# Kernel tuning notes

Measured on AMD Instinct MI355X. Metric: run time of the kernel, lower is better.

Reference implementation:

```python
import jax, jax.numpy as jnp
import numpy as np

LOG_2PIE = float(np.log(2 * np.pi * np.e))


def _mu_logvar(inputs, targets, W_fe, b_fe, W_lv, b_lv):
    # inputs: [Nep, N, Din], targets: [Nep, N, 1]
    phis = jax.nn.relu(jnp.einsum('end,df->enf', inputs, W_fe) + b_fe)  # [Nep, N, D]
    x = jnp.concatenate([targets, phis], axis=-1)                        # [Nep, N, D+1]
    # z = cat(mean over shots, std over shots (unbiased, as torch.std))
    z = jnp.concatenate([jnp.mean(x, axis=1), jnp.std(x, axis=1, ddof=1)], axis=-1)  # [Nep, T]
    mu = z  # use_net_for_mu=False
    logvar = jnp.clip(z @ W_lv + b_lv, -9.0, -2.0)  # Linear + Hardtanh(-9,-2)
    return mu, logvar


def _pairwise_kl(mu1, lv1, mu2, lv2):
    # KL(N(mu1_i, lv1_i) || N(mu2_j, lv2_j)) for all (i, j): [Nep, Nep]
    m1, l1 = mu1[:, None, :], lv1[:, None, :]
    m2, l2 = mu2[None, :, :], lv2[None, :, :]
    t = l2 - l1 + (jnp.exp(l1) + (m1 - m2) ** 2) * jnp.exp(-l2) - 1.0
    return 0.5 * jnp.sum(t, axis=-1)


def reference(train_inputs, train_targets, test_inputs, test_targets, W_fe, b_fe, W_lv, b_lv):
    mu_tr, lv_tr = _mu_logvar(train_inputs, train_targets, W_fe, b_fe, W_lv, b_lv)
    mu_te, lv_te = _mu_logvar(test_inputs, test_targets, W_fe, b_fe, W_lv, b_lv)
    T = mu_tr.shape[-1]
    # normal_entropy as written in source: logvar.sum() + 0.5*d*log(2*pi*e)
    H_tr = jnp.sum(lv_tr, axis=-1) + 0.5 * T * LOG_2PIE  # [Nep]
    H_te = jnp.sum(lv_te, axis=-1) + 0.5 * T * LOG_2PIE  # [Nep]
    score = (_pairwise_kl(mu_tr, lv_tr, mu_te, lv_te)
             + _pairwise_kl(mu_te, lv_te, mu_tr, lv_tr).T
             + H_tr[:, None] + H_te[None, :])
    probs = jax.nn.log_softmax(-score, axis=1)
    classes = jnp.arange(score.shape[0], dtype=jnp.int64 if jax.config.jax_enable_x64 else jnp.int32)
    return probs, classes


def setup_inputs() -> dict:
    key = jax.random.key(0)
    ks = jax.random.split(key, 6)
    Nep, N, Din, D = 256, 32, 512, 512
    T = 2 * (D + 1)
    return {
        'train_inputs': jax.random.normal(ks[0], (Nep, N, Din), jnp.float32),
        'train_targets': jax.random.normal(ks[1], (Nep, N, 1), jnp.float32),
        'test_inputs': jax.random.normal(ks[2], (Nep, N, Din), jnp.float32),
        'test_targets': jax.random.normal(ks[3], (Nep, N, 1), jnp.float32),
        'W_fe': jax.random.normal(ks[4], (Din, D), jnp.float32) / np.sqrt(Din),
        'b_fe': jnp.zeros((D,), jnp.float32),
        'W_lv': jax.random.normal(ks[5], (T, T), jnp.float32) / np.sqrt(T),
        'b_lv': jnp.zeros((T,), jnp.float32),
    }
```

## Files before the change

kernel.cpp:

```cpp
#include <hip/hip_runtime.h>
#include <math.h>

#define TDIM 1026
#define KP 1056
#define NP 1152
#define KSPLIT 7
#define KK 4224

typedef __attribute__((ext_vector_type(8))) short bf16x8;
typedef __attribute__((ext_vector_type(4))) float f32x4;

__device__ inline unsigned int pk_bf16(float a, float b) {
    unsigned int ua = __float_as_uint(a), ub = __float_as_uint(b);
    ua = (ua + 0x7FFFu + ((ua >> 16) & 1u)) >> 16;
    ub = (ub + 0x7FFFu + ((ub >> 16) & 1u)) & 0xFFFF0000u;
    return ua | ub;
}
__device__ inline unsigned short f2bf(float a) {
    unsigned int ua = __float_as_uint(a);
    return (unsigned short)((ua + 0x7FFFu + ((ua >> 16) & 1u)) >> 16);
}

__global__ __launch_bounds__(256)
void k_cvtboth(const float* __restrict__ Wfe, const float* __restrict__ Wlv,
               unsigned short* __restrict__ Wt, unsigned short* __restrict__ Wlt)
{
    __shared__ float T[32][33];
    const int z = blockIdx.z;
    if (z && (blockIdx.x >= 16 || blockIdx.y >= 16)) return;
    const float* W = z ? Wfe : Wlv;
    unsigned short* D = z ? Wt : Wlt;
    const int S  = z ? 512 : TDIM;
    const int DS = z ? 512 : KP;
    const int n0 = blockIdx.x * 32, k0 = blockIdx.y * 32;
    const int t = threadIdx.x;
    {
        int ky = t >> 3, nx = (t & 7) * 4;
#pragma unroll
        for (int i = 0; i < 4; ++i) {
            float v = 0.f;
            if (k0 + ky < S && n0 + nx + i < S)
                v = W[(size_t)(k0 + ky) * S + n0 + nx + i];
            T[nx + i][ky] = v;
        }
    }
    __syncthreads();
    {
        int ny = t >> 3, kx = (t & 7) * 4;
        ushort4 o;
        o.x = f2bf(T[ny][kx + 0]); o.y = f2bf(T[ny][kx + 1]);
        o.z = f2bf(T[ny][kx + 2]); o.w = f2bf(T[ny][kx + 3]);
        *(ushort4*)(D + (size_t)(n0 + ny) * DS + k0 + kx) = o;
    }
}

__global__ __launch_bounds__(256)
void k_fe_mfma(const float* __restrict__ Atr, const float* __restrict__ Ate,
               const unsigned short* __restrict__ Wt,
               const float* __restrict__ bfe, float* __restrict__ Z,
               unsigned short* __restrict__ Zb)
{
    __shared__ unsigned short As[64 * 40];
    __shared__ unsigned short Bs[128 * 40];
    __shared__ float2 sbuf[2 * 128];

    const int tid  = threadIdx.x;
    const int lane = tid & 63;
    const int wave = tid >> 6;
    const int m = lane & 15, quad = lane >> 4;
    const int row0 = blockIdx.x * 64;
    const int col0 = blockIdx.y * 128;
    const float* A = (row0 < 8192) ? Atr : Ate;
    const int ar0 = row0 & 8191;

    f32x4 acc[4][2];
#pragma unroll
    for (int i = 0; i < 4; ++i)
#pragma unroll
        for (int j = 0; j < 2; ++j) acc[i][j] = (f32x4){0.f, 0.f, 0.f, 0.f};

    const int srA = tid >> 2, skA = tid & 3;
    const int srB = tid >> 1, skB = tid & 1;

    float4 pa0, pa1;
    uint4  pb0, pb1;

#define FE_PRELOAD(K0)                                                          \
    {                                                                           \
        const float* ap = A + (size_t)(ar0 + srA) * 512 + (K0) + skA * 8;       \
        pa0 = *(const float4*)(ap);                                             \
        pa1 = *(const float4*)(ap + 4);                                         \
        const unsigned short* bp = Wt + (size_t)(col0 + srB) * 512 + (K0) + skB * 16; \
        pb0 = *(const uint4*)(bp);                                              \
        pb1 = *(const uint4*)(bp + 8);                                          \
    }

    FE_PRELOAD(0)
    for (int k0 = 0; k0 < 512; k0 += 32) {
        __syncthreads();
        {
            uint4 va;
            va.x = pk_bf16(pa0.x, pa0.y); va.y = pk_bf16(pa0.z, pa0.w);
            va.z = pk_bf16(pa1.x, pa1.y); va.w = pk_bf16(pa1.z, pa1.w);
            *(uint4*)(As + srA * 40 + skA * 8) = va;
            *(uint4*)(Bs + srB * 40 + skB * 16)     = pb0;
            *(uint4*)(Bs + srB * 40 + skB * 16 + 8) = pb1;
        }
        __syncthreads();
        if (k0 + 32 < 512) FE_PRELOAD(k0 + 32)
        bf16x8 af[4], bfr[2];
#pragma unroll
        for (int ti = 0; ti < 4; ++ti)
            af[ti] = *(const bf16x8*)(As + (ti * 16 + m) * 40 + quad * 8);
#pragma unroll
        for (int tj = 0; tj < 2; ++tj)
            bfr[tj] = *(const bf16x8*)(Bs + (wave * 32 + tj * 16 + m) * 40 + quad * 8);
#pragma unroll
        for (int ti = 0; ti < 4; ++ti)
#pragma unroll
            for (int tj = 0; tj < 2; ++tj)
                acc[ti][tj] = __builtin_amdgcn_mfma_f32_16x16x32_bf16(
                    af[ti], bfr[tj], acc[ti][tj], 0, 0, 0);
    }

#pragma unroll
    for (int ep = 0; ep < 2; ++ep) {
#pragma unroll
        for (int tj = 0; tj < 2; ++tj) {
            int colL = wave * 32 + tj * 16 + m;
            float b = bfe[col0 + colL];
            float s1 = 0.f, s2 = 0.f;
#pragma unroll
            for (int p = 0; p < 2; ++p) {
                int ti = ep * 2 + p;
#pragma unroll
                for (int r = 0; r < 4; ++r) {
                    float v = fmaxf(acc[ti][tj][r] + b, 0.f);
                    s1 += v; s2 += v * v;
                }
            }
            s1 += __shfl_xor(s1, 16); s1 += __shfl_xor(s1, 32);
            s2 += __shfl_xor(s2, 16); s2 += __shfl_xor(s2, 32);
            if (lane < 16) sbuf[ep * 128 + colL] = make_float2(s1, s2);
        }
    }
    __syncthreads();
    {
        int ep = tid >> 7, cl = tid & 127;
        float2 pr = sbuf[ep * 128 + cl];
        float mean = pr.x * (1.f / 32.f);
        float var  = (pr.y - 32.f * mean * mean) * (1.f / 31.f);
        float sd   = sqrtf(fmaxf(var, 0.f));
        int e = blockIdx.x * 2 + ep;
        int f = col0 + cl;
        Z[(size_t)e * TDIM + 1 + f]   = mean;
        Z[(size_t)e * TDIM + 514 + f] = sd;
        Zb[(size_t)e * KP + 1 + f]    = f2bf(mean);
        Zb[(size_t)e * KP + 514 + f]  = f2bf(sd);
    }
}

__global__ __launch_bounds__(256)
void k_tgt(const float* __restrict__ Ttr, const float* __restrict__ Tte,
           float* __restrict__ Z, unsigned short* __restrict__ Zb,
           float* __restrict__ Hs_te, float* __restrict__ cterm)
{
    if (blockIdx.x == 0) { Hs_te[threadIdx.x] = 0.f; cterm[threadIdx.x] = 0.f; }
    int e = blockIdx.x * 256 + threadIdx.x;
    if (e >= 512) return;
    const float* p = (e < 256) ? (Ttr + (size_t)e * 32) : (Tte + (size_t)(e - 256) * 32);
    float S1 = 0.f, S2 = 0.f;
#pragma unroll
    for (int n = 0; n < 32; ++n) { float v = p[n]; S1 += v; S2 += v * v; }
    float mean = S1 * (1.f / 32.f);
    float var  = (S2 - 32.f * mean * mean) * (1.f / 31.f);
    float sd   = sqrtf(fmaxf(var, 0.f));
    Z[(size_t)e * TDIM + 0]   = mean;
    Z[(size_t)e * TDIM + 513] = sd;
    Zb[(size_t)e * KP + 0]    = f2bf(mean);
    Zb[(size_t)e * KP + 513]  = f2bf(sd);
#pragma unroll
    for (int c = TDIM; c < KP; ++c) Zb[(size_t)e * KP + c] = 0;
}

__global__ __launch_bounds__(256)
void k_lv_mfma(const unsigned short* __restrict__ Zb,
               const unsigned short* __restrict__ Wlt,
               float* __restrict__ Cacc)
{
    __shared__ unsigned short As[128 * 40];
    __shared__ unsigned short Bs[128 * 40];

    const int tid  = threadIdx.x;
    const int lane = tid & 63;
    const int wave = tid >> 6;
    const int wr = wave >> 1, wc = wave & 1;
    const int m = lane & 15, quad = lane >> 4;
    const int col0 = blockIdx.x * 128;
    const int row0 = blockIdx.y * 128;
    const int p    = blockIdx.z;
    const int it0  = (p < 5) ? p * 5 : 25 + (p - 5) * 4;
    const int itn  = (p < 5) ? 5 : 4;

    f32x4 acc[4][4];
#pragma unroll
    for (int i = 0; i < 4; ++i)
#pragma unroll
        for (int j = 0; j < 4; ++j) acc[i][j] = (f32x4){0.f, 0.f, 0.f, 0.f};

    const int srow = tid >> 2;
    const int skc  = tid & 3;

    for (int it = it0; it < it0 + itn; ++it) {
        int k0 = it * 32;
#pragma unroll
        for (int s = 0; s < 2; ++s) {
            int row = srow + s * 64;
            uint4 va = *(const uint4*)(Zb  + (size_t)(row0 + row) * KP + k0 + skc * 8);
            uint4 vb = *(const uint4*)(Wlt + (size_t)(col0 + row) * KP + k0 + skc * 8);
            *(uint4*)(As + row * 40 + skc * 8) = va;
            *(uint4*)(Bs + row * 40 + skc * 8) = vb;
        }
        __syncthreads();
        bf16x8 af[4], bfr[4];
#pragma unroll
        for (int t2 = 0; t2 < 4; ++t2) {
            af[t2]  = *(const bf16x8*)(As + (wr * 64 + t2 * 16 + m) * 40 + quad * 8);
            bfr[t2] = *(const bf16x8*)(Bs + (wc * 64 + t2 * 16 + m) * 40 + quad * 8);
        }
#pragma unroll
        for (int ti = 0; ti < 4; ++ti)
#pragma unroll
            for (int tj = 0; tj < 4; ++tj)
                acc[ti][tj] = __builtin_amdgcn_mfma_f32_16x16x32_bf16(
                    af[ti], bfr[tj], acc[ti][tj], 0, 0, 0);
        __syncthreads();
    }

    float* C = Cacc + (size_t)p * 512 * NP;
#pragma unroll
    for (int ti = 0; ti < 4; ++ti)
#pragma unroll
        for (int tj = 0; tj < 4; ++tj) {
            int c = col0 + wc * 64 + tj * 16 + m;
#pragma unroll
            for (int r = 0; r < 4; ++r) {
                int rg = row0 + wr * 64 + ti * 16 + quad * 4 + r;
                C[(size_t)rg * NP + c] = acc[ti][tj][r];
            }
        }
}

__global__ __launch_bounds__(256)
void k_lv_ep(const float* __restrict__ Cacc, const float* __restrict__ Zf,
             const float* __restrict__ blv,
             unsigned short* __restrict__ Xb, unsigned short* __restrict__ Yb,
             float* __restrict__ Hs_te, float* __restrict__ cterm)
{
    const int t = threadIdx.x;
    const int rl = t >> 3;
    const int ci = t & 7;
    const int r  = blockIdx.y * 32 + rl;
    const int c0 = blockIdx.x * 32 + ci * 4;
    const bool is_te = (r >= 256);

    float4 s = make_float4(0.f, 0.f, 0.f, 0.f);
#pragma unroll
    for (int p = 0; p < KSPLIT; ++p) {
        float4 v = *(const float4*)(Cacc + (size_t)p * 512 * NP + (size_t)r * NP + c0);
        s.x += v.x; s.y += v.y; s.z += v.z; s.w += v.w;
    }
    float sv[4] = {s.x, s.y, s.z, s.w};

    unsigned short* O = is_te ? (Yb + (size_t)(r - 256) * KK) : (Xb + (size_t)r * KK);
    float h = 0.f, ct = 0.f;
#pragma unroll
    for (int q = 0; q < 4; ++q) {
        int c = c0 + q;
        bool cok = (c < TDIM);
        ushort4 o = make_ushort4(0, 0, 0, 0);
        if (cok) {
            float x = fminf(fmaxf(sv[q] + blv[c], -9.f), -2.f);
            float E = expf(x);
            float R = expf(-x);
            float mm = Zf[(size_t)r * TDIM + c];
            if (!is_te) {
                o.x = f2bf(E + mm * mm);
                o.y = f2bf(R);
                o.z = f2bf(-2.f * mm * R);
                o.w = f2bf(-2.f * mm);
            } else {
                o.x = f2bf(R);
                o.y = f2bf(E + mm * mm);
                o.z = f2bf(mm);
                o.w = f2bf(mm * R);
                h  += x;
                ct += mm * mm * R;
            }
        }
        *(ushort4*)(O + 4 * c) = o;
    }
    if (is_te) {
        h  += __shfl_xor(h, 1);  h  += __shfl_xor(h, 2);  h  += __shfl_xor(h, 4);
        ct += __shfl_xor(ct, 1); ct += __shfl_xor(ct, 2); ct += __shfl_xor(ct, 4);
        if (ci == 0) {
            atomicAdd(Hs_te + (r - 256), h);
            atomicAdd(cterm + (r - 256), ct);
        }
    }
}

__global__ __launch_bounds__(256)
void k_pgemm(const unsigned short* __restrict__ Xb,
             const unsigned short* __restrict__ Yb,
             float* __restrict__ Sp)
{
    __shared__ unsigned short As[128 * 40];
    __shared__ unsigned short Bs[128 * 40];

    const int tid  = threadIdx.x;
    const int lane = tid & 63;
    const int wave = tid >> 6;
    const int wr = wave >> 1, wc = wave & 1;
    const int m = lane & 15, quad = lane >> 4;
    const int col0 = blockIdx.x * 128;
    const int row0 = blockIdx.y * 128;
    const int p    = blockIdx.z;
    const int it0  = (p < 4) ? p * 9 : 36 + (p - 4) * 8;
    const int itn  = (p < 4) ? 9 : 8;

    f32x4 acc[4][4];
#pragma unroll
    for (int i = 0; i < 4; ++i)
#pragma unroll
        for (int j = 0; j < 4; ++j) acc[i][j] = (f32x4){0.f, 0.f, 0.f, 0.f};

    const int srow = tid >> 2;
    const int skc  = tid & 3;

    for (int it = it0; it < it0 + itn; ++it) {
        int k0 = it * 32;
#pragma unroll
        for (int s = 0; s < 2; ++s) {
            int row = srow + s * 64;
            uint4 va = *(const uint4*)(Xb + (size_t)(row0 + row) * KK + k0 + skc * 8);
            uint4 vb = *(const uint4*)(Yb + (size_t)(col0 + row) * KK + k0 + skc * 8);
            *(uint4*)(As + row * 40 + skc * 8) = va;
            *(uint4*)(Bs + row * 40 + skc * 8) = vb;
        }
        __syncthreads();
        bf16x8 af[4], bfr[4];
#pragma unroll
        for (int t2 = 0; t2 < 4; ++t2) {
            af[t2]  = *(const bf16x8*)(As + (wr * 64 + t2 * 16 + m) * 40 + quad * 8);
            bfr[t2] = *(const bf16x8*)(Bs + (wc * 64 + t2 * 16 + m) * 40 + quad * 8);
        }
#pragma unroll
        for (int ti = 0; ti < 4; ++ti)
#pragma unroll
            for (int tj = 0; tj < 4; ++tj)
                acc[ti][tj] = __builtin_amdgcn_mfma_f32_16x16x32_bf16(
                    af[ti], bfr[tj], acc[ti][tj], 0, 0, 0);
        __syncthreads();
    }

    float* C = Sp + (size_t)p * 65536;
#pragma unroll
    for (int ti = 0; ti < 4; ++ti)
#pragma unroll
        for (int tj = 0; tj < 4; ++tj) {
            int c = col0 + wc * 64 + tj * 16 + m;
#pragma unroll
            for (int r = 0; r < 4; ++r) {
                int rg = row0 + wr * 64 + ti * 16 + quad * 4 + r;
                C[(size_t)rg * 256 + c] = acc[ti][tj][r];
            }
        }
}

__global__ __launch_bounds__(256)
void k_soft(const float* __restrict__ Sp, const float* __restrict__ Hs_te,
            const float* __restrict__ cterm, float* __restrict__ outp)
{
    __shared__ float red[4], red2[4];
    const int i = blockIdx.x, j = threadIdx.x;
    float s = 0.f;
#pragma unroll
    for (int tc = 0; tc < 16; ++tc)
        s += Sp[((size_t)tc * 256 + i) * 256 + j];
    float v = -(0.5f * (s + cterm[j]) + Hs_te[j]);

    float m = v;
#pragma unroll
    for (int o = 32; o > 0; o >>= 1) m = fmaxf(m, __shfl_xor(m, o));
    if ((j & 63) == 0) red[j >> 6] = m;
    __syncthreads();
    m = fmaxf(fmaxf(red[0], red[1]), fmaxf(red[2], red[3]));

    float p = v - m;
    float t = expf(p);
#pragma unroll
    for (int o = 32; o > 0; o >>= 1) t += __shfl_xor(t, o);
    if ((j & 63) == 0) red2[j >> 6] = t;
    __syncthreads();
    t = red2[0] + red2[1] + red2[2] + red2[3];

    outp[(size_t)i * 256 + j] = p - logf(t);
    if (i == 0) outp[65536 + j] = (float)j;
}

__global__ __launch_bounds__(256)
void k_fe_f32(const float* __restrict__ Atr, const float* __restrict__ Ate,
              const float* __restrict__ Wfe, const float* __restrict__ bfe,
              float* __restrict__ Z, float* __restrict__ muT_te)
{
    __shared__ float lds[4224];
    float* Ast = lds;
    float* Bs  = lds + 2112;
    const int tid = threadIdx.x;
    const int tx = tid & 15;
    const int ty = tid >> 4;
    const int col0 = blockIdx.x * 128;
    const int row0 = blockIdx.y * 128;
    const float* A = (row0 < 8192) ? Atr : Ate;
    const int ar0 = (row0 < 8192) ? row0 : (row0 - 8192);

    float acc[8][8];
#pragma unroll
    for (int i = 0; i < 8; ++i)
#pragma unroll
        for (int j = 0; j < 8; ++j) acc[i][j] = 0.f;

    for (int k0 = 0; k0 < 512; k0 += 16) {
#pragma unroll
        for (int s = 0; s < 2; ++s) {
            int u = tid + s * 256;
            int row = u >> 2, q = u & 3;
            float4 v = *(const float4*)(A + (size_t)(ar0 + row) * 512 + k0 + q * 4);
            Ast[(q * 4 + 0) * 132 + row] = v.x;
            Ast[(q * 4 + 1) * 132 + row] = v.y;
            Ast[(q * 4 + 2) * 132 + row] = v.z;
            Ast[(q * 4 + 3) * 132 + row] = v.w;
        }
#pragma unroll
        for (int s = 0; s < 2; ++s) {
            int u = tid + s * 256;
            int kk = u >> 5, c8 = u & 31;
            float4 v = *(const float4*)(Wfe + (size_t)(k0 + kk) * 512 + col0 + c8 * 4);
            *(float4*)(Bs + kk * 132 + c8 * 4) = v;
        }
        __syncthreads();
#pragma unroll
        for (int kk = 0; kk < 16; ++kk) {
            float4 a0 = *(const float4*)(Ast + kk * 132 + ty * 8);
            float4 a1 = *(const float4*)(Ast + kk * 132 + ty * 8 + 4);
            float4 b0 = *(const float4*)(Bs + kk * 132 + tx * 4);
            float4 b1 = *(const float4*)(Bs + kk * 132 + 64 + tx * 4);
            float av[8] = {a0.x, a0.y, a0.z, a0.w, a1.x, a1.y, a1.z, a1.w};
            float bv[8] = {b0.x, b0.y, b0.z, b0.w, b1.x, b1.y, b1.z, b1.w};
#pragma unroll
            for (int i = 0; i < 8; ++i)
#pragma unroll
                for (int j = 0; j < 8; ++j)
                    acc[i][j] = fmaf(av[i], bv[j], acc[i][j]);
        }
        __syncthreads();
    }

    float2* sbuf = (float2*)lds;
#pragma unroll
    for (int j = 0; j < 8; ++j) {
        int cl = (j < 4) ? (tx * 4 + j) : (64 + tx * 4 + (j - 4));
        float b = bfe[col0 + cl];
        float s1 = 0.f, s2 = 0.f;
#pragma unroll
        for (int i = 0; i < 8; ++i) {
            float v = acc[i][j] + b;
            v = fmaxf(v, 0.f);
            s1 += v; s2 += v * v;
        }
        sbuf[ty * 128 + cl] = make_float2(s1, s2);
    }
    __syncthreads();
    for (int idx = tid; idx < 512; idx += 256) {
        int ep = idx >> 7, cl = idx & 127;
        float S1 = 0.f, S2 = 0.f;
#pragma unroll
        for (int q = 0; q < 4; ++q) {
            float2 p = sbuf[(ep * 4 + q) * 128 + cl];
            S1 += p.x; S2 += p.y;
        }
        float mean = S1 * (1.f / 32.f);
        float var  = (S2 - 32.f * mean * mean) * (1.f / 31.f);
        float sd   = sqrtf(fmaxf(var, 0.f));
        int e = (row0 >> 5) + ep;
        int f = col0 + cl;
        Z[(size_t)e * TDIM + 1 + f]   = mean;
        Z[(size_t)e * TDIM + 514 + f] = sd;
        if (e >= 256) {
            int j2 = e - 256;
            muT_te[(size_t)(1 + f) * 256 + j2]   = mean;
            muT_te[(size_t)(514 + f) * 256 + j2] = sd;
        }
    }
}

__global__ __launch_bounds__(256)
void k_tgt_f32(const float* __restrict__ Ttr, const float* __restrict__ Tte,
               float* __restrict__ Z, float* __restrict__ muT_te,
               float* __restrict__ Hs_te)
{
    if (blockIdx.x == 0) Hs_te[threadIdx.x] = 0.f;
    int e = blockIdx.x * 256 + threadIdx.x;
    if (e >= 512) return;
    const float* p = (e < 256) ? (Ttr + (size_t)e * 32) : (Tte + (size_t)(e - 256) * 32);
    float S1 = 0.f, S2 = 0.f;
#pragma unroll
    for (int n = 0; n < 32; ++n) { float v = p[n]; S1 += v; S2 += v * v; }
    float mean = S1 * (1.f / 32.f);
    float var  = (S2 - 32.f * mean * mean) * (1.f / 31.f);
    float sd   = sqrtf(fmaxf(var, 0.f));
    Z[(size_t)e * TDIM + 0]   = mean;
    Z[(size_t)e * TDIM + 513] = sd;
    if (e >= 256) {
        muT_te[(size_t)0 * 256 + (e - 256)]   = mean;
        muT_te[(size_t)513 * 256 + (e - 256)] = sd;
    }
}

__global__ __launch_bounds__(256)
void k_lv(const float* __restrict__ Z, const float* __restrict__ Wlv,
          const float* __restrict__ blv,
          float* __restrict__ E_tr, float* __restrict__ R_tr,
          float* __restrict__ E_teT, float* __restrict__ R_teT,
          float* __restrict__ Hs_te)
{
    __shared__ float Ast[16 * 68];
    __shared__ float Bs[16 * 68];
    const int tid = threadIdx.x;
    const int tx = tid & 15;
    const int ty = tid >> 4;
    const int col0 = blockIdx.x * 64;
    const int row0 = blockIdx.y * 64;

    float acc[4][4];
#pragma unroll
    for (int i = 0; i < 4; ++i)
#pragma unroll
        for (int j = 0; j < 4; ++j) acc[i][j] = 0.f;

    for (int k0 = 0; k0 < TDIM; k0 += 16) {
        {
            int row = tid >> 2, kp = tid & 3;
            const float* src = Z + (size_t)(row0 + row) * TDIM + k0 + kp * 4;
            float x0 = 0.f, x1 = 0.f, x2 = 0.f, x3 = 0.f;
            if (k0 + kp * 4 + 1 < TDIM) { float2 v = *(const float2*)(src);     x0 = v.x; x1 = v.y; }
            if (k0 + kp * 4 + 3 < TDIM) { float2 v = *(const float2*)(src + 2); x2 = v.x; x3 = v.y; }
            Ast[(kp * 4 + 0) * 68 + row] = x0;
            Ast[(kp * 4 + 1) * 68 + row] = x1;
            Ast[(kp * 4 + 2) * 68 + row] = x2;
            Ast[(kp * 4 + 3) * 68 + row] = x3;
        }
        {
            int kk = tid >> 4, cg = tid & 15;
#pragma unroll
            for (int c = 0; c < 4; ++c) {
                int col = col0 + cg * 4 + c;
                float v = 0.f;
                if (k0 + kk < TDIM && col < TDIM)
                    v = Wlv[(size_t)(k0 + kk) * TDIM + col];
                Bs[kk * 68 + cg * 4 + c] = v;
            }
        }
        __syncthreads();
#pragma unroll
        for (int kk = 0; kk < 16; ++kk) {
            float4 a = *(const float4*)(Ast + kk * 68 + ty * 4);
            float4 b = *(const float4*)(Bs + kk * 68 + tx * 4);
            float av[4] = {a.x, a.y, a.z, a.w};
            float bv[4] = {b.x, b.y, b.z, b.w};
#pragma unroll
            for (int i = 0; i < 4; ++i)
#pragma unroll
                for (int j = 0; j < 4; ++j)
                    acc[i][j] = fmaf(av[i], bv[j], acc[i][j]);
        }
        __syncthreads();
    }

    float hpart[4] = {0.f, 0.f, 0.f, 0.f};
#pragma unroll
    for (int i = 0; i < 4; ++i) {
        int r = row0 + ty * 4 + i;
#pragma unroll
        for (int j = 0; j < 4; ++j) {
            int c = col0 + tx * 4 + j;
            if (c < TDIM) {
                float lv = acc[i][j] + blv[c];
                lv = fminf(fmaxf(lv, -9.f), -2.f);
                float E = expf(lv);
                float R = expf(-lv);
                if (r < 256) {
                    E_tr[(size_t)r * TDIM + c] = E;
                    R_tr[(size_t)r * TDIM + c] = R;
                } else {
                    E_teT[(size_t)c * 256 + (r - 256)] = E;
                    R_teT[(size_t)c * 256 + (r - 256)] = R;
                    hpart[i] += lv;
                }
            }
        }
    }
    if (row0 >= 256) {
        __syncthreads();
        float* hbuf = Ast;
#pragma unroll
        for (int i = 0; i < 4; ++i) hbuf[(ty * 4 + i) * 16 + tx] = hpart[i];
        __syncthreads();
        if (tid < 64) {
            float s = 0.f;
#pragma unroll
            for (int x = 0; x < 16; ++x) s += hbuf[tid * 16 + x];
            atomicAdd(Hs_te + (row0 - 256 + tid), s);
        }
    }
}

#define TCH 65
__global__ __launch_bounds__(256)
void k_pair(const float* __restrict__ Z, const float* __restrict__ E_tr,
            const float* __restrict__ R_tr, const float* __restrict__ muT_te,
            const float* __restrict__ E_teT, const float* __restrict__ R_teT,
            float* __restrict__ Sp)
{
    __shared__ float Lm[8 * 68], Le[8 * 68], Lr[8 * 68];
    const int tid = threadIdx.x;
    const int i0 = blockIdx.x * 8;
    const int t0 = blockIdx.y * TCH;
    const int tlen = min(TCH, TDIM - t0);

    if (tid < tlen) {
#pragma unroll
        for (int r = 0; r < 8; ++r) {
            size_t off = (size_t)(i0 + r) * TDIM + t0 + tid;
            Lm[r * 68 + tid] = Z[off];
            Le[r * 68 + tid] = E_tr[off];
            Lr[r * 68 + tid] = R_tr[off];
        }
    }
    __syncthreads();

    float S[8];
#pragma unroll
    for (int r = 0; r < 8; ++r) S[r] = 0.f;
    const int j = tid;
    for (int tt = 0; tt < tlen; ++tt) {
        size_t o = (size_t)(t0 + tt) * 256 + j;
        float m2 = muT_te[o], e2 = E_teT[o], r2 = R_teT[o];
#pragma unroll
        for (int r = 0; r < 8; ++r) {
            float m1 = Lm[r * 68 + tt];
            float e1 = Le[r * 68 + tt];
            float r1 = Lr[r * 68 + tt];
            float d = m1 - m2;
            S[r] += e1 * r2 + e2 * r1 + d * d * (r1 + r2);
        }
    }
#pragma unroll
    for (int r = 0; r < 8; ++r)
        Sp[((size_t)blockIdx.y * 256 + i0 + r) * 256 + j] = S[r];
}

__global__ __launch_bounds__(256)
void k_soft_fb(const float* __restrict__ Sp, const float* __restrict__ Hs_te,
               float* __restrict__ outp)
{
    __shared__ float red[4], red2[4];
    const int i = blockIdx.x, j = threadIdx.x;
    float s = 0.f;
#pragma unroll
    for (int tc = 0; tc < 16; ++tc)
        s += Sp[((size_t)tc * 256 + i) * 256 + j];
    float v = -(0.5f * s + Hs_te[j]);

    float m = v;
#pragma unroll
    for (int o = 32; o > 0; o >>= 1) m = fmaxf(m, __shfl_xor(m, o));
    if ((j & 63) == 0) red[j >> 6] = m;
    __syncthreads();
    m = fmaxf(fmaxf(red[0], red[1]), fmaxf(red[2], red[3]));

    float p = v - m;
    float t = expf(p);
#pragma unroll
    for (int o = 32; o > 0; o >>= 1) t += __shfl_xor(t, o);
    if ((j & 63) == 0) red2[j >> 6] = t;
    __syncthreads();
    t = red2[0] + red2[1] + red2[2] + red2[3];

    outp[(size_t)i * 256 + j] = p - logf(t);
    if (i == 0) outp[65536 + j] = (float)j;
}

extern "C" void kernel_launch(void* const* d_in, const int* in_sizes, int n_in,
                              void* d_out, int out_size, void* d_ws, size_t ws_size,
                              hipStream_t stream)
{
    const float* tri = (const float*)d_in[0];
    const float* trt = (const float*)d_in[1];
    const float* tei = (const float*)d_in[2];
    const float* tet = (const float*)d_in[3];
    const float* Wfe = (const float*)d_in[4];
    const float* bfe = (const float*)d_in[5];
    const float* Wlv = (const float*)d_in[6];
    const float* blv = (const float*)d_in[7];
    float* outp = (float*)d_out;

    char* base = (char*)d_ws;
    float* Z     = (float*)base;
    float* Sp    = (float*)(base + 2101248);
    float* Hs_te = (float*)(base + 2101248 + 4194304);
    float* cterm = (float*)(base + 2101248 + 4194304 + 1024);
    float* Cacc  = (float*)(base + 6296576 + 1024);
    unsigned short* Wt = (unsigned short*)(base + 6297600 + 16515072);
    unsigned short* Xb = (unsigned short*)(base + 22812672 + 524288);
    unsigned short* Yb = (unsigned short*)(base + 23336960 + 2162688);
    unsigned short* Wlt = (unsigned short*)Sp;
    unsigned short* Zb  = (unsigned short*)((char*)Sp + 2433024);

    const size_t need = 23336960ull + 2162688ull + 2162688ull;
    const bool fast = (ws_size >= need);

    if (fast) {
        k_cvtboth<<<dim3(36, 33, 2), 256, 0, stream>>>(Wfe, Wlv, Wt, Wlt);
        k_fe_mfma<<<dim3(256, 4), 256, 0, stream>>>(tri, tei, Wt, bfe, Z, Zb);
        k_tgt    <<<2, 256, 0, stream>>>(trt, tet, Z, Zb, Hs_te, cterm);
        k_lv_mfma<<<dim3(9, 4, KSPLIT), 256, 0, stream>>>(Zb, Wlt, Cacc);
        k_lv_ep  <<<dim3(33, 16), 256, 0, stream>>>(Cacc, Z, blv, Xb, Yb, Hs_te, cterm);
        k_pgemm  <<<dim3(2, 2, 16), 256, 0, stream>>>(Xb, Yb, Sp);
        k_soft   <<<256, 256, 0, stream>>>(Sp, Hs_te, cterm, outp);
    } else {
        float* Zf    = (float*)d_ws;
        float* E_tr  = Zf + (size_t)512 * TDIM;
        float* R_tr  = E_tr + (size_t)256 * TDIM;
        float* muT   = R_tr + (size_t)256 * TDIM;
        float* E_teT = muT + (size_t)TDIM * 256;
        float* R_teT = E_teT + (size_t)TDIM * 256;
        float* Hs    = R_teT + (size_t)TDIM * 256;
        float* Spf   = Hs + 256;
        k_fe_f32 <<<dim3(4, 128), 256, 0, stream>>>(tri, tei, Wfe, bfe, Zf, muT);
        k_tgt_f32<<<2, 256, 0, stream>>>(trt, tet, Zf, muT, Hs);
        k_lv     <<<dim3(17, 8), 256, 0, stream>>>(Zf, Wlv, blv, E_tr, R_tr, E_teT, R_teT, Hs);
        k_pair   <<<dim3(32, 16), 256, 0, stream>>>(Zf, E_tr, R_tr, muT, E_teT, R_teT, Spf);
        k_soft_fb<<<256, 256, 0, stream>>>(Spf, Hs, outp);
    }
}
```

Before: 144.0 us.

## Double-buffer LDS in feature GEMM and fold target stats into convert kernel

The feature-extraction GEMM now keeps two LDS tile buffers, so each iteration stores the next tile while computing on the current one, needing one barrier per step instead of two. The small target-statistics kernel is merged into the weight-convert kernel as an extra grid z-slice, which removes one launch. This costs double the LDS for the GEMM tiles and launches many blocks that exit immediately.

```diff
diff --git a/kernel.cpp b/kernel.cpp
--- a/kernel.cpp
+++ b/kernel.cpp
@@ -23,17 +23,39 @@
 
 __global__ __launch_bounds__(256)
 void k_cvtboth(const float* __restrict__ Wfe, const float* __restrict__ Wlv,
-               unsigned short* __restrict__ Wt, unsigned short* __restrict__ Wlt)
+               unsigned short* __restrict__ Wt, unsigned short* __restrict__ Wlt,
+               const float* __restrict__ Ttr, const float* __restrict__ Tte,
+               float* __restrict__ Z, unsigned short* __restrict__ Zb,
+               float* __restrict__ Hs_te, float* __restrict__ cterm)
 {
     __shared__ float T[32][33];
     const int z = blockIdx.z;
+    const int t = threadIdx.x;
+    if (z == 2) {
+        if (blockIdx.y != 0 || blockIdx.x >= 2) return;
+        if (blockIdx.x == 0) { Hs_te[t] = 0.f; cterm[t] = 0.f; }
+        int e = blockIdx.x * 256 + t;
+        const float* p = (e < 256) ? (Ttr + (size_t)e * 32) : (Tte + (size_t)(e - 256) * 32);
+        float S1 = 0.f, S2 = 0.f;
+#pragma unroll
+        for (int n = 0; n < 32; ++n) { float v = p[n]; S1 += v; S2 += v * v; }
+        float mean = S1 * (1.f / 32.f);
+        float var  = (S2 - 32.f * mean * mean) * (1.f / 31.f);
+        float sd   = sqrtf(fmaxf(var, 0.f));
+        Z[(size_t)e * TDIM + 0]   = mean;
+        Z[(size_t)e * TDIM + 513] = sd;
+        Zb[(size_t)e * KP + 0]    = f2bf(mean);
+        Zb[(size_t)e * KP + 513]  = f2bf(sd);
+#pragma unroll
+        for (int c = TDIM; c < KP; ++c) Zb[(size_t)e * KP + c] = 0;
+        return;
+    }
     if (z && (blockIdx.x >= 16 || blockIdx.y >= 16)) return;
     const float* W = z ? Wfe : Wlv;
     unsigned short* D = z ? Wt : Wlt;
     const int S  = z ? 512 : TDIM;
     const int DS = z ? 512 : KP;
     const int n0 = blockIdx.x * 32, k0 = blockIdx.y * 32;
-    const int t = threadIdx.x;
     {
         int ky = t >> 3, nx = (t & 7) * 4;
 #pragma unroll
@@ -60,8 +82,8 @@
                const float* __restrict__ bfe, float* __restrict__ Z,
                unsigned short* __restrict__ Zb)
 {
-    __shared__ unsigned short As[64 * 40];
-    __shared__ unsigned short Bs[128 * 40];
+    __shared__ unsigned short As[2][64 * 40];
+    __shared__ unsigned short Bs[2][128 * 40];
     __shared__ float2 sbuf[2 * 128];
 
     const int tid  = threadIdx.x;
@@ -94,33 +116,42 @@
         pb0 = *(const uint4*)(bp);                                              \
         pb1 = *(const uint4*)(bp + 8);                                          \
     }
+#define FE_WRITE(BUF)                                                           \
+    {                                                                           \
+        uint4 va;                                                               \
+        va.x = pk_bf16(pa0.x, pa0.y); va.y = pk_bf16(pa0.z, pa0.w);             \
+        va.z = pk_bf16(pa1.x, pa1.y); va.w = pk_bf16(pa1.z, pa1.w);             \
+        *(uint4*)(As[BUF] + srA * 40 + skA * 8) = va;                           \
+        *(uint4*)(Bs[BUF] + srB * 40 + skB * 16)     = pb0;                     \
+        *(uint4*)(Bs[BUF] + srB * 40 + skB * 16 + 8) = pb1;                     \
+    }
 
     FE_PRELOAD(0)
+    FE_WRITE(0)
+    FE_PRELOAD(32)
+    __syncthreads();
+
+    int cur = 0;
     for (int k0 = 0; k0 < 512; k0 += 32) {
-        __syncthreads();
-        {
-            uint4 va;
-            va.x = pk_bf16(pa0.x, pa0.y); va.y = pk_bf16(pa0.z, pa0.w);
-            va.z = pk_bf16(pa1.x, pa1.y); va.w = pk_bf16(pa1.z, pa1.w);
-            *(uint4*)(As + srA * 40 + skA * 8) = va;
-            *(uint4*)(Bs + srB * 40 + skB * 16)     = pb0;
-            *(uint4*)(Bs + srB * 40 + skB * 16 + 8) = pb1;
-        }
-        __syncthreads();
-        if (k0 + 32 < 512) FE_PRELOAD(k0 + 32)
+        if (k0 + 32 < 512) {
+            FE_WRITE(cur ^ 1)
+            if (k0 + 64 < 512) FE_PRELOAD(k0 + 64)
+        }
         bf16x8 af[4], bfr[2];
 #pragma unroll
         for (int ti = 0; ti < 4; ++ti)
-            af[ti] = *(const bf16x8*)(As + (ti * 16 + m) * 40 + quad * 8);
+            af[ti] = *(const bf16x8*)(As[cur] + (ti * 16 + m) * 40 + quad * 8);
 #pragma unroll
         for (int tj = 0; tj < 2; ++tj)
-            bfr[tj] = *(const bf16x8*)(Bs + (wave * 32 + tj * 16 + m) * 40 + quad * 8);
+            bfr[tj] = *(const bf16x8*)(Bs[cur] + (wave * 32 + tj * 16 + m) * 40 + quad * 8);
 #pragma unroll
         for (int ti = 0; ti < 4; ++ti)
 #pragma unroll
             for (int tj = 0; tj < 2; ++tj)
                 acc[ti][tj] = __builtin_amdgcn_mfma_f32_16x16x32_bf16(
                     af[ti], bfr[tj], acc[ti][tj], 0, 0, 0);
+        __syncthreads();
+        cur ^= 1;
     }
 
 #pragma unroll
@@ -158,29 +189,6 @@
         Zb[(size_t)e * KP + 1 + f]    = f2bf(mean);
         Zb[(size_t)e * KP + 514 + f]  = f2bf(sd);
     }
-}
-
-__global__ __launch_bounds__(256)
-void k_tgt(const float* __restrict__ Ttr, const float* __restrict__ Tte,
-           float* __restrict__ Z, unsigned short* __restrict__ Zb,
-           float* __restrict__ Hs_te, float* __restrict__ cterm)
-{
-    if (blockIdx.x == 0) { Hs_te[threadIdx.x] = 0.f; cterm[threadIdx.x] = 0.f; }
-    int e = blockIdx.x * 256 + threadIdx.x;
-    if (e >= 512) return;
-    const float* p = (e < 256) ? (Ttr + (size_t)e * 32) : (Tte + (size_t)(e - 256) * 32);
-    float S1 = 0.f, S2 = 0.f;
-#pragma unroll
-    for (int n = 0; n < 32; ++n) { float v = p[n]; S1 += v; S2 += v * v; }
-    float mean = S1 * (1.f / 32.f);
-    float var  = (S2 - 32.f * mean * mean) * (1.f / 31.f);
-    float sd   = sqrtf(fmaxf(var, 0.f));
-    Z[(size_t)e * TDIM + 0]   = mean;
-    Z[(size_t)e * TDIM + 513] = sd;
-    Zb[(size_t)e * KP + 0]    = f2bf(mean);
-    Zb[(size_t)e * KP + 513]  = f2bf(sd);
-#pragma unroll
-    for (int c = TDIM; c < KP; ++c) Zb[(size_t)e * KP + c] = 0;
 }
 
 __global__ __launch_bounds__(256)
@@ -732,9 +740,9 @@
     const bool fast = (ws_size >= need);
 
     if (fast) {
-        k_cvtboth<<<dim3(36, 33, 2), 256, 0, stream>>>(Wfe, Wlv, Wt, Wlt);
+        k_cvtboth<<<dim3(36, 33, 3), 256, 0, stream>>>(Wfe, Wlv, Wt, Wlt,
+                                                       trt, tet, Z, Zb, Hs_te, cterm);
         k_fe_mfma<<<dim3(256, 4), 256, 0, stream>>>(tri, tei, Wt, bfe, Z, Zb);
-        k_tgt    <<<2, 256, 0, stream>>>(trt, tet, Z, Zb, Hs_te, cterm);
         k_lv_mfma<<<dim3(9, 4, KSPLIT), 256, 0, stream>>>(Zb, Wlt, Cacc);
         k_lv_ep  <<<dim3(33, 16), 256, 0, stream>>>(Cacc, Z, blv, Xb, Yb, Hs_te, cterm);
         k_pgemm  <<<dim3(2, 2, 16), 256, 0, stream>>>(Xb, Yb, Sp);
```

Measured after the change: 139.4 us (median of 3 runs). -3.2%, faster.
